# Optimization experiments

Hardware: AMD Instinct MI355X
Metric: run time of the kernel (lower is better)

## Reference

```python
import jax, jax.numpy as jnp
from jax import lax
import numpy as np

E = 16          # n_routed_experts
H = 2048        # hidden_size
I = 1408        # moe_intermediate_size
T = 2048        # tokens
K = 6           # top_k


def setup_inputs() -> dict:
    key = jax.random.key(0)
    k1, k2, k3, k4, k5 = jax.random.split(key, 5)
    hidden_states = jax.random.normal(k1, (T, H), dtype=jnp.float32)
    top_k_index = jax.random.randint(k2, (T, K), 0, E)
    top_k_weights = jax.random.uniform(k3, (T, K), dtype=jnp.float32)
    gate_up_proj = jax.random.normal(k4, (E, 2 * I, H), dtype=jnp.float32) * 0.02
    down_proj = jax.random.normal(k5, (E, H, I), dtype=jnp.float32) * 0.02
    return {
        "hidden_states": hidden_states,
        "top_k_index": top_k_index,
        "top_k_weights": top_k_weights,
        "gate_up_proj": gate_up_proj,
        "down_proj": down_proj,
    }


def reference(hidden_states, top_k_index, top_k_weights, gate_up_proj, down_proj):
    # combine[t, e] = sum over k-slots of top_k_weights[t, k] where top_k_index[t, k] == e
    # (scatter-add handles duplicate expert picks identically to index_add_).
    n_tok = hidden_states.shape[0]
    n_exp = gate_up_proj.shape[0]
    combine = jnp.zeros((n_tok, n_exp), hidden_states.dtype)
    combine = combine.at[jnp.arange(n_tok)[:, None], top_k_index].add(top_k_weights)

    def expert_step(acc, params):
        gu, dn, c_e = params  # gu: [2I, H], dn: [H, I], c_e: [n_tok]
        gate, up = jnp.split(hidden_states @ gu.T, 2, axis=-1)  # each [n_tok, I]
        y = (jax.nn.silu(gate) * up) @ dn.T                     # [n_tok, H]
        return acc + y * c_e[:, None], None

    out, _ = lax.scan(
        expert_step,
        jnp.zeros_like(hidden_states),
        (gate_up_proj, down_proj, combine.T),
    )
    return out
```

## Files before the change

kernel.cpp:

```cpp
#include <hip/hip_runtime.h>
#include <hip/hip_bf16.h>
#include <cstdint>

#define T_TOK 2048
#define HD 2048
#define ID 1408
#define NE 16
#define TOPK 6

#define BM 256
#define BK 64
#define BN 32
#define NT1 44
#define NT2 64
#define GMAX 64

typedef __bf16 bf16x8 __attribute__((ext_vector_type(8)));
typedef float f32x4 __attribute__((ext_vector_type(4)));

typedef const __attribute__((address_space(1))) void* gas1_t;
typedef __attribute__((address_space(3))) void* las3_t;
#define GLDS16(g, l) __builtin_amdgcn_global_load_lds((gas1_t)(g), (las3_t)(l), 16, 0, 0)


__global__ void k_combine(const int* __restrict__ idx, const float* __restrict__ w,
                          float* __restrict__ combine) {
    int t = blockIdx.x * blockDim.x + threadIdx.x;
    if (t >= T_TOK) return;
    int ie[TOPK];
    float fw[TOPK];
#pragma unroll
    for (int k = 0; k < TOPK; k++) { ie[k] = idx[t * TOPK + k]; fw[k] = w[t * TOPK + k]; }
#pragma unroll
    for (int e = 0; e < NE; e++) {
        float s = 0.f;
#pragma unroll
        for (int k = 0; k < TOPK; k++) if (ie[k] == e) s += fw[k];
        combine[t * NE + e] = s;
    }
}

__global__ void k_lists(const float* __restrict__ combine, int* __restrict__ counts,
                        int* __restrict__ tok, float* __restrict__ wts) {
    int t = blockIdx.x * blockDim.x + threadIdx.x;
    if (t >= T_TOK) return;
    for (int e = 0; e < NE; e++) {
        float c = combine[t * NE + e];
        if (c != 0.0f) {
            int p = atomicAdd(&counts[e], 1);
            tok[e * T_TOK + p] = t;
            wts[e * T_TOK + p] = c;
        }
    }
}

__global__ void k_cvt(const float* __restrict__ x, __bf16* __restrict__ xb) {
    int i = (blockIdx.x * 256 + threadIdx.x) * 8;
    float4 a = *(const float4*)(x + i);
    float4 b = *(const float4*)(x + i + 4);
    bf16x8 o;
    o[0] = (__bf16)a.x; o[1] = (__bf16)a.y; o[2] = (__bf16)a.z; o[3] = (__bf16)a.w;
    o[4] = (__bf16)b.x; o[5] = (__bf16)b.y; o[6] = (__bf16)b.z; o[7] = (__bf16)b.w;
    *(bf16x8*)(xb + i) = o;
}


__device__ __forceinline__ int swz(int row, int cb) {
    return row * 128 + (cb ^ ((row & 7) << 4));
}

__device__ __forceinline__ bf16x8 ldfrag(const __bf16* base, int row, int cb) {
    return *(const bf16x8*)((const char*)base + swz(row, cb));
}

__device__ __forceinline__ void stage8(const float* __restrict__ src, char* lds,
                                       int row, int cb) {
    float4 f0 = ((const float4*)src)[0];
    float4 f1 = ((const float4*)src)[1];
    bf16x8 o;
    o[0] = (__bf16)f0.x; o[1] = (__bf16)f0.y; o[2] = (__bf16)f0.z; o[3] = (__bf16)f0.w;
    o[4] = (__bf16)f1.x; o[5] = (__bf16)f1.y; o[6] = (__bf16)f1.z; o[7] = (__bf16)f1.w;
    *(bf16x8*)(lds + swz(row, cb)) = o;
}

__device__ __forceinline__ bool decode_item(const int* __restrict__ counts, int it,
                                            int ntn, int& e, int& m, int& n, int& cnt) {
    int r = it;
    for (int ee = 0; ee < NE; ee++) {
        int c = counts[ee];
        int nm = (c + BM - 1) >> 8;
        int tot = nm * ntn;
        if (r < tot) { e = ee; m = r % nm; n = r / nm; cnt = c; return true; }
        r -= tot;
    }
    return false;
}


__global__ __launch_bounds__(256, 4) void k_gemm1(
    const __bf16* __restrict__ Xb, const float* __restrict__ gup,
    const int* __restrict__ counts, const int* __restrict__ tok,
    __bf16* __restrict__ act) {
    __shared__ __align__(16) __bf16 sA[BM * BK];
    __shared__ __align__(16) __bf16 sBg[BN * BK];
    __shared__ __align__(16) __bf16 sBu[BN * BK];

    int e, m, n, cnt;
    if (!decode_item(counts, blockIdx.x, NT1, e, m, n, cnt)) return;
    int m0 = m * BM;
    int n0 = n * BN;

    int tid = threadIdx.x;
    int lane = tid & 63;
    int wid = tid >> 6;
    int l15 = lane & 15, lh = lane >> 4;
    int csw = ((lane & 7) ^ ((lane >> 3) & 7)) * 8;

    const __bf16* pA[8];
#pragma unroll
    for (int j = 0; j < 8; j++) {
        int r = 64 * wid + 8 * j + (lane >> 3);
        int g = m0 + r;
        if (g >= cnt) g = cnt - 1;
        pA[j] = Xb + (size_t)tok[e * T_TOK + g] * HD + csw;
    }

    int br = tid >> 3, bc = tid & 7;
    const float* gbase = gup + (size_t)e * (2 * ID) * HD;
    const float* bgSrc = gbase + (size_t)(n0 + br) * HD + bc * 8;
    const float* buSrc = gbase + (size_t)(ID + n0 + br) * HD + bc * 8;

    f32x4 accg[4][2] = {};
    f32x4 accu[4][2] = {};

    for (int k0 = 0; k0 < HD; k0 += BK) {
        __syncthreads();
#pragma unroll
        for (int j = 0; j < 8; j++)
            GLDS16(pA[j] + k0, &sA[(64 * wid + 8 * j) * BK]);
        stage8(bgSrc + k0, (char*)sBg, br, bc * 16);
        stage8(buSrc + k0, (char*)sBu, br, bc * 16);
        __syncthreads();
#pragma unroll
        for (int kk = 0; kk < 2; kk++) {
            int cb = kk * 64 + lh * 16;
            bf16x8 a[4];
#pragma unroll
            for (int fm = 0; fm < 4; fm++)
                a[fm] = ldfrag(sA, wid * 64 + fm * 16 + l15, cb);
#pragma unroll
            for (int fn = 0; fn < 2; fn++) {
                bf16x8 bg = ldfrag(sBg, fn * 16 + l15, cb);
                bf16x8 bu = ldfrag(sBu, fn * 16 + l15, cb);
#pragma unroll
                for (int fm = 0; fm < 4; fm++) {
                    accg[fm][fn] = __builtin_amdgcn_mfma_f32_16x16x32_bf16(a[fm], bg, accg[fm][fn], 0, 0, 0);
                    accu[fm][fn] = __builtin_amdgcn_mfma_f32_16x16x32_bf16(a[fm], bu, accu[fm][fn], 0, 0, 0);
                }
            }
        }
    }

#pragma unroll
    for (int fm = 0; fm < 4; fm++) {
#pragma unroll
        for (int fn = 0; fn < 2; fn++) {
#pragma unroll
            for (int j = 0; j < 4; j++) {
                int mloc = wid * 64 + fm * 16 + lh * 4 + j;
                int g = m0 + mloc;
                if (g < cnt) {
                    float gv = accg[fm][fn][j];
                    float uv = accu[fm][fn][j];
                    float sv = gv * (1.0f / (1.0f + __expf(-gv)));
                    int nn = n0 + fn * 16 + l15;
                    act[((size_t)e * T_TOK + g) * ID + nn] = (__bf16)(sv * uv);
                }
            }
        }
    }
}


__global__ __launch_bounds__(256, 4) void k_gemm2(
    const __bf16* __restrict__ act, const float* __restrict__ dn,
    const int* __restrict__ counts, const int* __restrict__ tok,
    const float* __restrict__ wts, float* __restrict__ out) {
    __shared__ __align__(16) __bf16 sA[BM * BK];
    __shared__ __align__(16) __bf16 sB[BN * BK];
    __shared__ int tokLds[BM];
    __shared__ float wtLds[BM];

    int e, m, n, cnt;
    if (!decode_item(counts, blockIdx.x, NT2, e, m, n, cnt)) return;
    int m0 = m * BM;
    int n0 = n * BN;

    int tid = threadIdx.x;
    int lane = tid & 63;
    int wid = tid >> 6;
    int l15 = lane & 15, lh = lane >> 4;
    int csw = ((lane & 7) ^ ((lane >> 3) & 7)) * 8;

    if (tid < BM) {
        int g = m0 + tid;
        bool v = g < cnt;
        tokLds[tid] = v ? tok[e * T_TOK + g] : 0;
        wtLds[tid] = v ? wts[e * T_TOK + g] : 0.f;
    }

    const __bf16* pA[8];
#pragma unroll
    for (int j = 0; j < 8; j++) {
        int r = 64 * wid + 8 * j + (lane >> 3);
        int g = m0 + r;
        if (g >= cnt) g = cnt - 1;
        pA[j] = act + ((size_t)e * T_TOK + g) * ID + csw;
    }

    int br = tid >> 3, bc = tid & 7;
    const float* bSrc = dn + (size_t)e * HD * ID + (size_t)(n0 + br) * ID + bc * 8;

    f32x4 acc[4][2] = {};

    for (int k0 = 0; k0 < ID; k0 += BK) {
        __syncthreads();
#pragma unroll
        for (int j = 0; j < 8; j++)
            GLDS16(pA[j] + k0, &sA[(64 * wid + 8 * j) * BK]);
        stage8(bSrc + k0, (char*)sB, br, bc * 16);
        __syncthreads();
#pragma unroll
        for (int kk = 0; kk < 2; kk++) {
            int cb = kk * 64 + lh * 16;
            bf16x8 a[4];
#pragma unroll
            for (int fm = 0; fm < 4; fm++)
                a[fm] = ldfrag(sA, wid * 64 + fm * 16 + l15, cb);
#pragma unroll
            for (int fn = 0; fn < 2; fn++) {
                bf16x8 b = ldfrag(sB, fn * 16 + l15, cb);
#pragma unroll
                for (int fm = 0; fm < 4; fm++)
                    acc[fm][fn] = __builtin_amdgcn_mfma_f32_16x16x32_bf16(a[fm], b, acc[fm][fn], 0, 0, 0);
            }
        }
    }

    __syncthreads();
#pragma unroll
    for (int fm = 0; fm < 4; fm++) {
#pragma unroll
        for (int fn = 0; fn < 2; fn++) {
#pragma unroll
            for (int j = 0; j < 4; j++) {
                int mloc = wid * 64 + fm * 16 + lh * 4 + j;
                int g = m0 + mloc;
                if (g < cnt) {
                    float v = acc[fm][fn][j] * wtLds[mloc];
                    int nn = n0 + fn * 16 + l15;
                    atomicAdd(&out[(size_t)tokLds[mloc] * HD + nn], v);
                }
            }
        }
    }
}


extern "C" void kernel_launch(void* const* d_in, const int* in_sizes, int n_in,
                              void* d_out, int out_size, void* d_ws, size_t ws_size,
                              hipStream_t stream) {
    const float* hs = (const float*)d_in[0];
    const int* tki = (const int*)d_in[1];
    const float* tkw = (const float*)d_in[2];
    const float* gup = (const float*)d_in[3];
    const float* dnp = (const float*)d_in[4];
    float* out = (float*)d_out;

    char* p = (char*)d_ws;
    int* counts = (int*)p;      p += 256;
    float* combine = (float*)p; p += (size_t)T_TOK * NE * 4;
    int* tok = (int*)p;         p += (size_t)NE * T_TOK * 4;
    float* wts = (float*)p;     p += (size_t)NE * T_TOK * 4;
    __bf16* Xb = (__bf16*)p;    p += (size_t)T_TOK * HD * 2;
    __bf16* act = (__bf16*)p;

    hipMemsetAsync(counts, 0, 256, stream);
    hipMemsetAsync(d_out, 0, (size_t)T_TOK * HD * 4, stream);
    k_combine<<<T_TOK / 256, 256, 0, stream>>>(tki, tkw, combine);
    k_lists<<<T_TOK / 256, 256, 0, stream>>>(combine, counts, tok, wts);
    k_cvt<<<(T_TOK * HD / 8) / 256, 256, 0, stream>>>(hs, Xb);
    k_gemm1<<<dim3(GMAX * NT1), 256, 0, stream>>>(Xb, gup, counts, tok, act);
    k_gemm2<<<dim3(GMAX * NT2), 256, 0, stream>>>(act, dnp, counts, tok, wts, out);
}
```

Baseline: 463.8 us.

## Pre-convert expert weights to bf16 and stream them via direct LDS loads

Adds a pass that converts the fp32 gate_up and down weights to bf16 in workspace before each GEMM, when the workspace is large enough. The GEMMs can then load weights with global_load_lds instead of per-thread fp32 loads followed by conversion and LDS stores. The trade-off is an extra full read of fp32 weights plus a bf16 write (about 277 MB fp32 total), and the GEMM tiles re-read the bf16 copy once per 256-token tile. The old fp32 GEMM paths are kept as a fallback when the workspace is too small.

```diff
diff --git a/kernel.cpp b/kernel.cpp
--- a/kernel.cpp
+++ b/kernel.cpp
@@ -64,6 +64,19 @@
     *(bf16x8*)(xb + i) = o;
 }
 
+__global__ void k_cvtw(const float* __restrict__ src, __bf16* __restrict__ dst, int n8) {
+    int stride = gridDim.x * blockDim.x;
+    for (int i = blockIdx.x * blockDim.x + threadIdx.x; i < n8; i += stride) {
+        size_t o = (size_t)i * 8;
+        float4 a = *(const float4*)(src + o);
+        float4 b = *(const float4*)(src + o + 4);
+        bf16x8 v;
+        v[0] = (__bf16)a.x; v[1] = (__bf16)a.y; v[2] = (__bf16)a.z; v[3] = (__bf16)a.w;
+        v[4] = (__bf16)b.x; v[5] = (__bf16)b.y; v[6] = (__bf16)b.z; v[7] = (__bf16)b.w;
+        *(bf16x8*)(dst + o) = v;
+    }
+}
+
 
 __device__ __forceinline__ int swz(int row, int cb) {
     return row * 128 + (cb ^ ((row & 7) << 4));
@@ -97,8 +110,8 @@
 }
 
 
-__global__ __launch_bounds__(256, 4) void k_gemm1(
-    const __bf16* __restrict__ Xb, const float* __restrict__ gup,
+__global__ __launch_bounds__(256, 4) void k_gemm1_bf16(
+    const __bf16* __restrict__ Xb, const __bf16* __restrict__ wgu,
     const int* __restrict__ counts, const int* __restrict__ tok,
     __bf16* __restrict__ act) {
     __shared__ __align__(16) __bf16 sA[BM * BK];
@@ -125,10 +138,11 @@
         pA[j] = Xb + (size_t)tok[e * T_TOK + g] * HD + csw;
     }
 
-    int br = tid >> 3, bc = tid & 7;
-    const float* gbase = gup + (size_t)e * (2 * ID) * HD;
-    const float* bgSrc = gbase + (size_t)(n0 + br) * HD + bc * 8;
-    const float* buSrc = gbase + (size_t)(ID + n0 + br) * HD + bc * 8;
+    int brow = 8 * wid + (lane >> 3);
+    int bsw = ((lane & 7) ^ (lane >> 3)) * 8;
+    const __bf16* wbase = wgu + (size_t)e * (2 * ID) * HD;
+    const __bf16* pBg = wbase + (size_t)(n0 + brow) * HD + bsw;
+    const __bf16* pBu = wbase + (size_t)(ID + n0 + brow) * HD + bsw;
 
     f32x4 accg[4][2] = {};
     f32x4 accu[4][2] = {};
@@ -138,8 +152,8 @@
 #pragma unroll
         for (int j = 0; j < 8; j++)
             GLDS16(pA[j] + k0, &sA[(64 * wid + 8 * j) * BK]);
-        stage8(bgSrc + k0, (char*)sBg, br, bc * 16);
-        stage8(buSrc + k0, (char*)sBu, br, bc * 16);
+        GLDS16(pBg + k0, &sBg[wid * 512]);
+        GLDS16(pBu + k0, &sBu[wid * 512]);
         __syncthreads();
 #pragma unroll
         for (int kk = 0; kk < 2; kk++) {
@@ -182,7 +196,178 @@
 }
 
 
-__global__ __launch_bounds__(256, 4) void k_gemm2(
+__global__ __launch_bounds__(256, 4) void k_gemm1_f32(
+    const __bf16* __restrict__ Xb, const float* __restrict__ gup,
+    const int* __restrict__ counts, const int* __restrict__ tok,
+    __bf16* __restrict__ act) {
+    __shared__ __align__(16) __bf16 sA[BM * BK];
+    __shared__ __align__(16) __bf16 sBg[BN * BK];
+    __shared__ __align__(16) __bf16 sBu[BN * BK];
+
+    int e, m, n, cnt;
+    if (!decode_item(counts, blockIdx.x, NT1, e, m, n, cnt)) return;
+    int m0 = m * BM;
+    int n0 = n * BN;
+
+    int tid = threadIdx.x;
+    int lane = tid & 63;
+    int wid = tid >> 6;
+    int l15 = lane & 15, lh = lane >> 4;
+    int csw = ((lane & 7) ^ ((lane >> 3) & 7)) * 8;
+
+    const __bf16* pA[8];
+#pragma unroll
+    for (int j = 0; j < 8; j++) {
+        int r = 64 * wid + 8 * j + (lane >> 3);
+        int g = m0 + r;
+        if (g >= cnt) g = cnt - 1;
+        pA[j] = Xb + (size_t)tok[e * T_TOK + g] * HD + csw;
+    }
+
+    int br = tid >> 3, bc = tid & 7;
+    const float* gbase = gup + (size_t)e * (2 * ID) * HD;
+    const float* bgSrc = gbase + (size_t)(n0 + br) * HD + bc * 8;
+    const float* buSrc = gbase + (size_t)(ID + n0 + br) * HD + bc * 8;
+
+    f32x4 accg[4][2] = {};
+    f32x4 accu[4][2] = {};
+
+    for (int k0 = 0; k0 < HD; k0 += BK) {
+        __syncthreads();
+#pragma unroll
+        for (int j = 0; j < 8; j++)
+            GLDS16(pA[j] + k0, &sA[(64 * wid + 8 * j) * BK]);
+        stage8(bgSrc + k0, (char*)sBg, br, bc * 16);
+        stage8(buSrc + k0, (char*)sBu, br, bc * 16);
+        __syncthreads();
+#pragma unroll
+        for (int kk = 0; kk < 2; kk++) {
+            int cb = kk * 64 + lh * 16;
+            bf16x8 a[4];
+#pragma unroll
+            for (int fm = 0; fm < 4; fm++)
+                a[fm] = ldfrag(sA, wid * 64 + fm * 16 + l15, cb);
+#pragma unroll
+            for (int fn = 0; fn < 2; fn++) {
+                bf16x8 bg = ldfrag(sBg, fn * 16 + l15, cb);
+                bf16x8 bu = ldfrag(sBu, fn * 16 + l15, cb);
+#pragma unroll
+                for (int fm = 0; fm < 4; fm++) {
+                    accg[fm][fn] = __builtin_amdgcn_mfma_f32_16x16x32_bf16(a[fm], bg, accg[fm][fn], 0, 0, 0);
+                    accu[fm][fn] = __builtin_amdgcn_mfma_f32_16x16x32_bf16(a[fm], bu, accu[fm][fn], 0, 0, 0);
+                }
+            }
+        }
+    }
+
+#pragma unroll
+    for (int fm = 0; fm < 4; fm++) {
+#pragma unroll
+        for (int fn = 0; fn < 2; fn++) {
+#pragma unroll
+            for (int j = 0; j < 4; j++) {
+                int mloc = wid * 64 + fm * 16 + lh * 4 + j;
+                int g = m0 + mloc;
+                if (g < cnt) {
+                    float gv = accg[fm][fn][j];
+                    float uv = accu[fm][fn][j];
+                    float sv = gv * (1.0f / (1.0f + __expf(-gv)));
+                    int nn = n0 + fn * 16 + l15;
+                    act[((size_t)e * T_TOK + g) * ID + nn] = (__bf16)(sv * uv);
+                }
+            }
+        }
+    }
+}
+
+
+__global__ __launch_bounds__(256, 4) void k_gemm2_bf16(
+    const __bf16* __restrict__ act, const __bf16* __restrict__ wdn,
+    const int* __restrict__ counts, const int* __restrict__ tok,
+    const float* __restrict__ wts, float* __restrict__ out) {
+    __shared__ __align__(16) __bf16 sA[BM * BK];
+    __shared__ __align__(16) __bf16 sB[BN * BK];
+    __shared__ int tokLds[BM];
+    __shared__ float wtLds[BM];
+
+    int e, m, n, cnt;
+    if (!decode_item(counts, blockIdx.x, NT2, e, m, n, cnt)) return;
+    int m0 = m * BM;
+    int n0 = n * BN;
+
+    int tid = threadIdx.x;
+    int lane = tid & 63;
+    int wid = tid >> 6;
+    int l15 = lane & 15, lh = lane >> 4;
+    int csw = ((lane & 7) ^ ((lane >> 3) & 7)) * 8;
+
+    if (tid < BM) {
+        int g = m0 + tid;
+        bool v = g < cnt;
+        tokLds[tid] = v ? tok[e * T_TOK + g] : 0;
+        wtLds[tid] = v ? wts[e * T_TOK + g] : 0.f;
+    }
+
+    const __bf16* pA[8];
+#pragma unroll
+    for (int j = 0; j < 8; j++) {
+        int r = 64 * wid + 8 * j + (lane >> 3);
+        int g = m0 + r;
+        if (g >= cnt) g = cnt - 1;
+        pA[j] = act + ((size_t)e * T_TOK + g) * ID + csw;
+    }
+
+    int brow = 8 * wid + (lane >> 3);
+    int bsw = ((lane & 7) ^ (lane >> 3)) * 8;
+    const __bf16* pB = wdn + ((size_t)e * HD + (n0 + brow)) * ID + bsw;
+
+    f32x4 acc[4][2] = {};
+
+    for (int k0 = 0; k0 < ID; k0 += BK) {
+        __syncthreads();
+#pragma unroll
+        for (int j = 0; j < 8; j++)
+            GLDS16(pA[j] + k0, &sA[(64 * wid + 8 * j) * BK]);
+        GLDS16(pB + k0, &sB[wid * 512]);
+        __syncthreads();
+#pragma unroll
+        for (int kk = 0; kk < 2; kk++) {
+            int cb = kk * 64 + lh * 16;
+            bf16x8 a[4];
+#pragma unroll
+            for (int fm = 0; fm < 4; fm++)
+                a[fm] = ldfrag(sA, wid * 64 + fm * 16 + l15, cb);
+#pragma unroll
+            for (int fn = 0; fn < 2; fn++) {
+                bf16x8 b = ldfrag(sB, fn * 16 + l15, cb);
+#pragma unroll
+                for (int fm = 0; fm < 4; fm++)
+                    acc[fm][fn] = __builtin_amdgcn_mfma_f32_16x16x32_bf16(a[fm], b, acc[fm][fn], 0, 0, 0);
+            }
+        }
+    }
+
+    __syncthreads();
+#pragma unroll
+    for (int fm = 0; fm < 4; fm++) {
+#pragma unroll
+        for (int fn = 0; fn < 2; fn++) {
+#pragma unroll
+            for (int j = 0; j < 4; j++) {
+                int mloc = wid * 64 + fm * 16 + lh * 4 + j;
+                int g = m0 + mloc;
+                if (g < cnt) {
+                    float v = acc[fm][fn][j] * wtLds[mloc];
+                    int nn = n0 + fn * 16 + l15;
+                    atomicAdd(&out[(size_t)tokLds[mloc] * HD + nn], v);
+                }
+            }
+        }
+    }
+}
+
+
+__global__ __launch_bounds__(256, 4) void k_gemm2_f32(
     const __bf16* __restrict__ act, const float* __restrict__ dn,
     const int* __restrict__ counts, const int* __restrict__ tok,
     const float* __restrict__ wts, float* __restrict__ out) {
@@ -277,19 +462,40 @@
     const float* dnp = (const float*)d_in[4];
     float* out = (float*)d_out;
 
+    const size_t nGU = (size_t)NE * (2 * ID) * HD;
+    const size_t nDN = (size_t)NE * HD * ID;
+
     char* p = (char*)d_ws;
     int* counts = (int*)p;      p += 256;
     float* combine = (float*)p; p += (size_t)T_TOK * NE * 4;
     int* tok = (int*)p;         p += (size_t)NE * T_TOK * 4;
     float* wts = (float*)p;     p += (size_t)NE * T_TOK * 4;
     __bf16* Xb = (__bf16*)p;    p += (size_t)T_TOK * HD * 2;
-    __bf16* act = (__bf16*)p;
+    __bf16* act = (__bf16*)p;   p += (size_t)NE * T_TOK * ID * 2;
+    size_t used_base = (size_t)(p - (char*)d_ws);
+    __bf16* wgu = (__bf16*)p;
+    __bf16* wdn = (__bf16*)(p + nGU * 2);
+
+    bool cvt_gu = ws_size >= used_base + nGU * 2;
+    bool cvt_dn = ws_size >= used_base + nGU * 2 + nDN * 2;
 
     hipMemsetAsync(counts, 0, 256, stream);
     hipMemsetAsync(d_out, 0, (size_t)T_TOK * HD * 4, stream);
     k_combine<<<T_TOK / 256, 256, 0, stream>>>(tki, tkw, combine);
     k_lists<<<T_TOK / 256, 256, 0, stream>>>(combine, counts, tok, wts);
     k_cvt<<<(T_TOK * HD / 8) / 256, 256, 0, stream>>>(hs, Xb);
-    k_gemm1<<<dim3(GMAX * NT1), 256, 0, stream>>>(Xb, gup, counts, tok, act);
-    k_gemm2<<<dim3(GMAX * NT2), 256, 0, stream>>>(act, dnp, counts, tok, wts, out);
-}
+
+    if (cvt_gu) {
+        k_cvtw<<<2048, 256, 0, stream>>>(gup, wgu, (int)(nGU / 8));
+        k_gemm1_bf16<<<dim3(GMAX * NT1), 256, 0, stream>>>(Xb, wgu, counts, tok, act);
+    } else {
+        k_gemm1_f32<<<dim3(GMAX * NT1), 256, 0, stream>>>(Xb, gup, counts, tok, act);
+    }
+
+    if (cvt_dn) {
+        k_cvtw<<<2048, 256, 0, stream>>>(dnp, wdn, (int)(nDN / 8));
+        k_gemm2_bf16<<<dim3(GMAX * NT2), 256, 0, stream>>>(act, wdn, counts, tok, wts, out);
+    } else {
+        k_gemm2_f32<<<dim3(GMAX * NT2), 256, 0, stream>>>(act, dnp, counts, tok, wts, out);
+    }
+}
```

New measurement: 507.8 us. 9.5% more time.

## Software-pipeline weight loads with double-buffered LDS in both expert GEMMs

Applied to the files above, without the earlier changes.

Both grouped GEMM kernels now prefetch the next K-tile of fp32 weights into registers while computing the current tile, and stage the B tiles into double-buffered LDS. Explicit waitcnt and raw barriers replace __syncthreads, so the A tile load is issued right after compute. gemm1 launch bounds drop to 3 waves per SIMD to allow more registers. gemm2 also drops the LDS token/weight table and reads tok and wts directly in the epilogue. The hand-written waitcnt counts are fragile, and the lower occupancy hint may reduce latency hiding.

```diff
diff --git a/kernel.cpp b/kernel.cpp
--- a/kernel.cpp
+++ b/kernel.cpp
@@ -21,6 +21,14 @@
 typedef const __attribute__((address_space(1))) void* gas1_t;
 typedef __attribute__((address_space(3))) void* las3_t;
 #define GLDS16(g, l) __builtin_amdgcn_global_load_lds((gas1_t)(g), (las3_t)(l), 16, 0, 0)
+
+__device__ __forceinline__ void bar() {
+    asm volatile("" ::: "memory");
+    __builtin_amdgcn_s_barrier();
+    asm volatile("" ::: "memory");
+}
+#define WAITV(N) asm volatile("s_waitcnt vmcnt(" #N ")" ::: "memory")
+#define WAITL0   asm volatile("s_waitcnt lgkmcnt(0)" ::: "memory")
 
 
 __global__ void k_combine(const int* __restrict__ idx, const float* __restrict__ w,
@@ -73,10 +81,7 @@
     return *(const bf16x8*)((const char*)base + swz(row, cb));
 }
 
-__device__ __forceinline__ void stage8(const float* __restrict__ src, char* lds,
-                                       int row, int cb) {
-    float4 f0 = ((const float4*)src)[0];
-    float4 f1 = ((const float4*)src)[1];
+__device__ __forceinline__ void stage8v(char* lds, int row, int cb, float4 f0, float4 f1) {
     bf16x8 o;
     o[0] = (__bf16)f0.x; o[1] = (__bf16)f0.y; o[2] = (__bf16)f0.z; o[3] = (__bf16)f0.w;
     o[4] = (__bf16)f1.x; o[5] = (__bf16)f1.y; o[6] = (__bf16)f1.z; o[7] = (__bf16)f1.w;
@@ -97,13 +102,13 @@
 }
 
 
-__global__ __launch_bounds__(256, 4) void k_gemm1(
+__global__ __launch_bounds__(256, 3) void k_gemm1(
     const __bf16* __restrict__ Xb, const float* __restrict__ gup,
     const int* __restrict__ counts, const int* __restrict__ tok,
     __bf16* __restrict__ act) {
     __shared__ __align__(16) __bf16 sA[BM * BK];
-    __shared__ __align__(16) __bf16 sBg[BN * BK];
-    __shared__ __align__(16) __bf16 sBu[BN * BK];
+    __shared__ __align__(16) __bf16 sBg[2][BN * BK];
+    __shared__ __align__(16) __bf16 sBu[2][BN * BK];
 
     int e, m, n, cnt;
     if (!decode_item(counts, blockIdx.x, NT1, e, m, n, cnt)) return;
@@ -133,14 +138,31 @@
     f32x4 accg[4][2] = {};
     f32x4 accu[4][2] = {};
 
-    for (int k0 = 0; k0 < HD; k0 += BK) {
-        __syncthreads();
-#pragma unroll
-        for (int j = 0; j < 8; j++)
-            GLDS16(pA[j] + k0, &sA[(64 * wid + 8 * j) * BK]);
-        stage8(bgSrc + k0, (char*)sBg, br, bc * 16);
-        stage8(buSrc + k0, (char*)sBu, br, bc * 16);
-        __syncthreads();
+    const int NT = HD / BK;
+
+    float4 g0 = ((const float4*)bgSrc)[0], g1 = ((const float4*)bgSrc)[1];
+    float4 u0 = ((const float4*)buSrc)[0], u1 = ((const float4*)buSrc)[1];
+#pragma unroll
+    for (int j = 0; j < 8; j++)
+        GLDS16(pA[j], &sA[(64 * wid + 8 * j) * BK]);
+    stage8v((char*)sBg[0], br, bc * 16, g0, g1);
+    stage8v((char*)sBu[0], br, bc * 16, u0, u1);
+    WAITL0;
+    bar();
+
+    for (int k = 0; k < NT; k++) {
+        int cur = k & 1, nxt = cur ^ 1;
+        int kn = (k + 1 < NT) ? (k + 1) : k;
+        {
+            const float* bg = bgSrc + kn * BK;
+            const float* bu = buSrc + kn * BK;
+            g0 = ((const float4*)bg)[0]; g1 = ((const float4*)bg)[1];
+            u0 = ((const float4*)bu)[0]; u1 = ((const float4*)bu)[1];
+        }
+        WAITV(4);
+        bar();
+        const __bf16* sBgc = sBg[cur];
+        const __bf16* sBuc = sBu[cur];
 #pragma unroll
         for (int kk = 0; kk < 2; kk++) {
             int cb = kk * 64 + lh * 16;
@@ -150,14 +172,23 @@
                 a[fm] = ldfrag(sA, wid * 64 + fm * 16 + l15, cb);
 #pragma unroll
             for (int fn = 0; fn < 2; fn++) {
-                bf16x8 bg = ldfrag(sBg, fn * 16 + l15, cb);
-                bf16x8 bu = ldfrag(sBu, fn * 16 + l15, cb);
+                bf16x8 bg = ldfrag(sBgc, fn * 16 + l15, cb);
+                bf16x8 bu = ldfrag(sBuc, fn * 16 + l15, cb);
 #pragma unroll
                 for (int fm = 0; fm < 4; fm++) {
                     accg[fm][fn] = __builtin_amdgcn_mfma_f32_16x16x32_bf16(a[fm], bg, accg[fm][fn], 0, 0, 0);
                     accu[fm][fn] = __builtin_amdgcn_mfma_f32_16x16x32_bf16(a[fm], bu, accu[fm][fn], 0, 0, 0);
                 }
             }
+        }
+        stage8v((char*)sBg[nxt], br, bc * 16, g0, g1);
+        stage8v((char*)sBu[nxt], br, bc * 16, u0, u1);
+        WAITL0;
+        bar();
+        if (k + 1 < NT) {
+#pragma unroll
+            for (int j = 0; j < 8; j++)
+                GLDS16(pA[j] + (k + 1) * BK, &sA[(64 * wid + 8 * j) * BK]);
         }
     }
 
@@ -187,9 +218,7 @@
     const int* __restrict__ counts, const int* __restrict__ tok,
     const float* __restrict__ wts, float* __restrict__ out) {
     __shared__ __align__(16) __bf16 sA[BM * BK];
-    __shared__ __align__(16) __bf16 sB[BN * BK];
-    __shared__ int tokLds[BM];
-    __shared__ float wtLds[BM];
+    __shared__ __align__(16) __bf16 sB[2][BN * BK];
 
     int e, m, n, cnt;
     if (!decode_item(counts, blockIdx.x, NT2, e, m, n, cnt)) return;
@@ -202,13 +231,6 @@
     int l15 = lane & 15, lh = lane >> 4;
     int csw = ((lane & 7) ^ ((lane >> 3) & 7)) * 8;
 
-    if (tid < BM) {
-        int g = m0 + tid;
-        bool v = g < cnt;
-        tokLds[tid] = v ? tok[e * T_TOK + g] : 0;
-        wtLds[tid] = v ? wts[e * T_TOK + g] : 0.f;
-    }
-
     const __bf16* pA[8];
 #pragma unroll
     for (int j = 0; j < 8; j++) {
@@ -223,13 +245,26 @@
 
     f32x4 acc[4][2] = {};
 
-    for (int k0 = 0; k0 < ID; k0 += BK) {
-        __syncthreads();
-#pragma unroll
-        for (int j = 0; j < 8; j++)
-            GLDS16(pA[j] + k0, &sA[(64 * wid + 8 * j) * BK]);
-        stage8(bSrc + k0, (char*)sB, br, bc * 16);
-        __syncthreads();
+    const int NT = ID / BK;
+
+    float4 b0 = ((const float4*)bSrc)[0], b1 = ((const float4*)bSrc)[1];
+#pragma unroll
+    for (int j = 0; j < 8; j++)
+        GLDS16(pA[j], &sA[(64 * wid + 8 * j) * BK]);
+    stage8v((char*)sB[0], br, bc * 16, b0, b1);
+    WAITL0;
+    bar();
+
+    for (int k = 0; k < NT; k++) {
+        int cur = k & 1, nxt = cur ^ 1;
+        int kn = (k + 1 < NT) ? (k + 1) : k;
+        {
+            const float* bs = bSrc + kn * BK;
+            b0 = ((const float4*)bs)[0]; b1 = ((const float4*)bs)[1];
+        }
+        WAITV(2);
+        bar();
+        const __bf16* sBc = sB[cur];
 #pragma unroll
         for (int kk = 0; kk < 2; kk++) {
             int cb = kk * 64 + lh * 16;
@@ -239,27 +274,35 @@
                 a[fm] = ldfrag(sA, wid * 64 + fm * 16 + l15, cb);
 #pragma unroll
             for (int fn = 0; fn < 2; fn++) {
-                bf16x8 b = ldfrag(sB, fn * 16 + l15, cb);
+                bf16x8 b = ldfrag(sBc, fn * 16 + l15, cb);
 #pragma unroll
                 for (int fm = 0; fm < 4; fm++)
                     acc[fm][fn] = __builtin_amdgcn_mfma_f32_16x16x32_bf16(a[fm], b, acc[fm][fn], 0, 0, 0);
             }
         }
-    }
-
-    __syncthreads();
+        stage8v((char*)sB[nxt], br, bc * 16, b0, b1);
+        WAITL0;
+        bar();
+        if (k + 1 < NT) {
+#pragma unroll
+            for (int j = 0; j < 8; j++)
+                GLDS16(pA[j] + (k + 1) * BK, &sA[(64 * wid + 8 * j) * BK]);
+        }
+    }
+
 #pragma unroll
     for (int fm = 0; fm < 4; fm++) {
 #pragma unroll
-        for (int fn = 0; fn < 2; fn++) {
-#pragma unroll
-            for (int j = 0; j < 4; j++) {
-                int mloc = wid * 64 + fm * 16 + lh * 4 + j;
-                int g = m0 + mloc;
-                if (g < cnt) {
-                    float v = acc[fm][fn][j] * wtLds[mloc];
+        for (int j = 0; j < 4; j++) {
+            int mloc = wid * 64 + fm * 16 + lh * 4 + j;
+            int g = m0 + mloc;
+            if (g < cnt) {
+                int t = tok[e * T_TOK + g];
+                float w = wts[e * T_TOK + g];
+#pragma unroll
+                for (int fn = 0; fn < 2; fn++) {
                     int nn = n0 + fn * 16 + l15;
-                    atomicAdd(&out[(size_t)tokLds[mloc] * HD + nn], v);
+                    atomicAdd(&out[(size_t)t * HD + nn], acc[fm][fn][j] * w);
                 }
             }
         }
```

Result: slower. 552.6 us (+19.2%).

## Double-buffer LDS tiles with BK=32 and prefetch next tile in both GEMMs

Applied to the files above, without the earlier changes.

Both expert GEMM kernels now use two LDS buffers with a K-tile of 32. The next tile's activation rows are issued via global_load_lds and the weight floats are loaded into registers before the current tile's MFMAs, then converted and stored after them, leaving one barrier per iteration. This is meant to hide global load latency behind matrix math. The swizzle is adapted to the 64-byte rows, and the down-projection epilogue reads token and weight indices straight from global memory instead of staging them in LDS. The cost is twice as many loop iterations with half the math per barrier, plus extra registers for the prefetched values.

```diff
diff --git a/kernel.cpp b/kernel.cpp
--- a/kernel.cpp
+++ b/kernel.cpp
@@ -9,7 +9,7 @@
 #define TOPK 6
 
 #define BM 256
-#define BK 64
+#define BK 32
 #define BN 32
 #define NT1 44
 #define NT2 64
@@ -65,22 +65,19 @@
 }
 
 
-__device__ __forceinline__ int swz(int row, int cb) {
-    return row * 128 + (cb ^ ((row & 7) << 4));
-}
-
-__device__ __forceinline__ bf16x8 ldfrag(const __bf16* base, int row, int cb) {
-    return *(const bf16x8*)((const char*)base + swz(row, cb));
-}
-
-__device__ __forceinline__ void stage8(const float* __restrict__ src, char* lds,
-                                       int row, int cb) {
-    float4 f0 = ((const float4*)src)[0];
-    float4 f1 = ((const float4*)src)[1];
+__device__ __forceinline__ int swz32(int row, int cb) {
+    return row * 64 + (cb ^ (((row >> 1) & 3) << 4));
+}
+
+__device__ __forceinline__ bf16x8 ldfrag32(const __bf16* base, int row, int cb) {
+    return *(const bf16x8*)((const char*)base + swz32(row, cb));
+}
+
+__device__ __forceinline__ void stage8v32(char* lds, int row, int q, float4 f0, float4 f1) {
     bf16x8 o;
     o[0] = (__bf16)f0.x; o[1] = (__bf16)f0.y; o[2] = (__bf16)f0.z; o[3] = (__bf16)f0.w;
     o[4] = (__bf16)f1.x; o[5] = (__bf16)f1.y; o[6] = (__bf16)f1.z; o[7] = (__bf16)f1.w;
-    *(bf16x8*)(lds + swz(row, cb)) = o;
+    *(bf16x8*)(lds + swz32(row, q << 4)) = o;
 }
 
 __device__ __forceinline__ bool decode_item(const int* __restrict__ counts, int it,
@@ -101,9 +98,9 @@
     const __bf16* __restrict__ Xb, const float* __restrict__ gup,
     const int* __restrict__ counts, const int* __restrict__ tok,
     __bf16* __restrict__ act) {
-    __shared__ __align__(16) __bf16 sA[BM * BK];
-    __shared__ __align__(16) __bf16 sBg[BN * BK];
-    __shared__ __align__(16) __bf16 sBu[BN * BK];
+    __shared__ __align__(16) __bf16 sA[2][BM * BK];
+    __shared__ __align__(16) __bf16 sBg[2][BN * BK];
+    __shared__ __align__(16) __bf16 sBu[2][BN * BK];
 
     int e, m, n, cnt;
     if (!decode_item(counts, blockIdx.x, NT1, e, m, n, cnt)) return;
@@ -114,51 +111,76 @@
     int lane = tid & 63;
     int wid = tid >> 6;
     int l15 = lane & 15, lh = lane >> 4;
-    int csw = ((lane & 7) ^ ((lane >> 3) & 7)) * 8;
-
-    const __bf16* pA[8];
-#pragma unroll
-    for (int j = 0; j < 8; j++) {
-        int r = 64 * wid + 8 * j + (lane >> 3);
+
+    const __bf16* pA[4];
+    int csw = ((lane & 3) ^ ((lane >> 3) & 3)) * 8;
+#pragma unroll
+    for (int j = 0; j < 4; j++) {
+        int r = 64 * wid + 16 * j + (lane >> 2);
         int g = m0 + r;
         if (g >= cnt) g = cnt - 1;
         pA[j] = Xb + (size_t)tok[e * T_TOK + g] * HD + csw;
     }
 
-    int br = tid >> 3, bc = tid & 7;
+    int t4 = tid & 127;
+    int brow = t4 >> 2, bq = t4 & 3;
     const float* gbase = gup + (size_t)e * (2 * ID) * HD;
-    const float* bgSrc = gbase + (size_t)(n0 + br) * HD + bc * 8;
-    const float* buSrc = gbase + (size_t)(ID + n0 + br) * HD + bc * 8;
+    const float* bSrc = (tid < 128)
+        ? gbase + (size_t)(n0 + brow) * HD + bq * 8
+        : gbase + (size_t)(ID + n0 + brow) * HD + bq * 8;
 
     f32x4 accg[4][2] = {};
     f32x4 accu[4][2] = {};
 
-    for (int k0 = 0; k0 < HD; k0 += BK) {
+    const int NT = HD / BK;
+
+    {
+        float4 b0 = ((const float4*)bSrc)[0], b1 = ((const float4*)bSrc)[1];
+#pragma unroll
+        for (int j = 0; j < 4; j++)
+            GLDS16(pA[j], &sA[0][(64 * wid + 16 * j) * BK]);
+        char* dst = (tid < 128) ? (char*)sBg[0] : (char*)sBu[0];
+        stage8v32(dst, brow, bq, b0, b1);
+    }
+    __syncthreads();
+
+    for (int k = 0; k < NT; k++) {
+        int cur = k & 1, nxt = cur ^ 1;
+        bool pf = (k + 1 < NT);
+        float4 b0, b1;
+        if (pf) {
+            int k0 = (k + 1) * BK;
+#pragma unroll
+            for (int j = 0; j < 4; j++)
+                GLDS16(pA[j] + k0, &sA[nxt][(64 * wid + 16 * j) * BK]);
+            const float* bs = bSrc + k0;
+            b0 = ((const float4*)bs)[0]; b1 = ((const float4*)bs)[1];
+        }
+
+        const __bf16* sAc = sA[cur];
+        const __bf16* sBgc = sBg[cur];
+        const __bf16* sBuc = sBu[cur];
+        int cb = lh * 16;
+        bf16x8 a[4];
+#pragma unroll
+        for (int fm = 0; fm < 4; fm++)
+            a[fm] = ldfrag32(sAc, wid * 64 + fm * 16 + l15, cb);
+#pragma unroll
+        for (int fn = 0; fn < 2; fn++) {
+            bf16x8 bg = ldfrag32(sBgc, fn * 16 + l15, cb);
+            bf16x8 bu = ldfrag32(sBuc, fn * 16 + l15, cb);
+#pragma unroll
+            for (int fm = 0; fm < 4; fm++) {
+                accg[fm][fn] = __builtin_amdgcn_mfma_f32_16x16x32_bf16(a[fm], bg, accg[fm][fn], 0, 0, 0);
+                accu[fm][fn] = __builtin_amdgcn_mfma_f32_16x16x32_bf16(a[fm], bu, accu[fm][fn], 0, 0, 0);
+            }
+        }
+
+        if (pf) {
+            char* dst = (tid < 128) ? (char*)sBg[nxt] : (char*)sBu[nxt];
+            stage8v32(dst, brow, bq, b0, b1);
+        }
         __syncthreads();
-#pragma unroll
-        for (int j = 0; j < 8; j++)
-            GLDS16(pA[j] + k0, &sA[(64 * wid + 8 * j) * BK]);
-        stage8(bgSrc + k0, (char*)sBg, br, bc * 16);
-        stage8(buSrc + k0, (char*)sBu, br, bc * 16);
-        __syncthreads();
-#pragma unroll
-        for (int kk = 0; kk < 2; kk++) {
-            int cb = kk * 64 + lh * 16;
-            bf16x8 a[4];
-#pragma unroll
-            for (int fm = 0; fm < 4; fm++)
-                a[fm] = ldfrag(sA, wid * 64 + fm * 16 + l15, cb);
-#pragma unroll
-            for (int fn = 0; fn < 2; fn++) {
-                bf16x8 bg = ldfrag(sBg, fn * 16 + l15, cb);
-                bf16x8 bu = ldfrag(sBu, fn * 16 + l15, cb);
-#pragma unroll
-                for (int fm = 0; fm < 4; fm++) {
-                    accg[fm][fn] = __builtin_amdgcn_mfma_f32_16x16x32_bf16(a[fm], bg, accg[fm][fn], 0, 0, 0);
-                    accu[fm][fn] = __builtin_amdgcn_mfma_f32_16x16x32_bf16(a[fm], bu, accu[fm][fn], 0, 0, 0);
-                }
-            }
-        }
     }
 
 #pragma unroll
@@ -186,10 +208,8 @@
     const __bf16* __restrict__ act, const float* __restrict__ dn,
     const int* __restrict__ counts, const int* __restrict__ tok,
     const float* __restrict__ wts, float* __restrict__ out) {
-    __shared__ __align__(16) __bf16 sA[BM * BK];
-    __shared__ __align__(16) __bf16 sB[BN * BK];
-    __shared__ int tokLds[BM];
-    __shared__ float wtLds[BM];
+    __shared__ __align__(16) __bf16 sA[2][BM * BK];
+    __shared__ __align__(16) __bf16 sB[2][BN * BK];
 
     int e, m, n, cnt;
     if (!decode_item(counts, blockIdx.x, NT2, e, m, n, cnt)) return;
@@ -200,66 +220,82 @@
     int lane = tid & 63;
     int wid = tid >> 6;
     int l15 = lane & 15, lh = lane >> 4;
-    int csw = ((lane & 7) ^ ((lane >> 3) & 7)) * 8;
-
-    if (tid < BM) {
-        int g = m0 + tid;
-        bool v = g < cnt;
-        tokLds[tid] = v ? tok[e * T_TOK + g] : 0;
-        wtLds[tid] = v ? wts[e * T_TOK + g] : 0.f;
-    }
-
-    const __bf16* pA[8];
-#pragma unroll
-    for (int j = 0; j < 8; j++) {
-        int r = 64 * wid + 8 * j + (lane >> 3);
+
+    const __bf16* pA[4];
+    int csw = ((lane & 3) ^ ((lane >> 3) & 3)) * 8;
+#pragma unroll
+    for (int j = 0; j < 4; j++) {
+        int r = 64 * wid + 16 * j + (lane >> 2);
         int g = m0 + r;
         if (g >= cnt) g = cnt - 1;
         pA[j] = act + ((size_t)e * T_TOK + g) * ID + csw;
     }
 
-    int br = tid >> 3, bc = tid & 7;
-    const float* bSrc = dn + (size_t)e * HD * ID + (size_t)(n0 + br) * ID + bc * 8;
+    int t4 = tid & 127;
+    int brow = t4 >> 2, bq = t4 & 3;
+    const float* bSrc = dn + (size_t)e * HD * ID + (size_t)(n0 + brow) * ID + bq * 8;
 
     f32x4 acc[4][2] = {};
 
-    for (int k0 = 0; k0 < ID; k0 += BK) {
+    const int NT = ID / BK;
+
+    {
+        float4 b0, b1;
+        if (tid < 128) { b0 = ((const float4*)bSrc)[0]; b1 = ((const float4*)bSrc)[1]; }
+#pragma unroll
+        for (int j = 0; j < 4; j++)
+            GLDS16(pA[j], &sA[0][(64 * wid + 16 * j) * BK]);
+        if (tid < 128) stage8v32((char*)sB[0], brow, bq, b0, b1);
+    }
+    __syncthreads();
+
+    for (int k = 0; k < NT; k++) {
+        int cur = k & 1, nxt = cur ^ 1;
+        bool pf = (k + 1 < NT);
+        float4 b0, b1;
+        if (pf) {
+            int k0 = (k + 1) * BK;
+#pragma unroll
+            for (int j = 0; j < 4; j++)
+                GLDS16(pA[j] + k0, &sA[nxt][(64 * wid + 16 * j) * BK]);
+            if (tid < 128) {
+                const float* bs = bSrc + k0;
+                b0 = ((const float4*)bs)[0]; b1 = ((const float4*)bs)[1];
+            }
+        }
+
+        const __bf16* sAc = sA[cur];
+        const __bf16* sBc = sB[cur];
+        int cb = lh * 16;
+        bf16x8 a[4];
+#pragma unroll
+        for (int fm = 0; fm < 4; fm++)
+            a[fm] = ldfrag32(sAc, wid * 64 + fm * 16 + l15, cb);
+#pragma unroll
+        for (int fn = 0; fn < 2; fn++) {
+            bf16x8 b = ldfrag32(sBc, fn * 16 + l15, cb);
+#pragma unroll
+            for (int fm = 0; fm < 4; fm++)
+                acc[fm][fn] = __builtin_amdgcn_mfma_f32_16x16x32_bf16(a[fm], b, acc[fm][fn], 0, 0, 0);
+        }
+
+        if (pf && tid < 128) stage8v32((char*)sB[nxt], brow, bq, b0, b1);
         __syncthreads();
-#pragma unroll
-        for (int j = 0; j < 8; j++)
-            GLDS16(pA[j] + k0, &sA[(64 * wid + 8 * j) * BK]);
-        stage8(bSrc + k0, (char*)sB, br, bc * 16);
-        __syncthreads();
-#pragma unroll
-        for (int kk = 0; kk < 2; kk++) {
-            int cb = kk * 64 + lh * 16;
-            bf16x8 a[4];
-#pragma unroll
-            for (int fm = 0; fm < 4; fm++)
-                a[fm] = ldfrag(sA, wid * 64 + fm * 16 + l15, cb);
-#pragma unroll
-            for (int fn = 0; fn < 2; fn++) {
-                bf16x8 b = ldfrag(sB, fn * 16 + l15, cb);
-#pragma unroll
-                for (int fm = 0; fm < 4; fm++)
-                    acc[fm][fn] = __builtin_amdgcn_mfma_f32_16x16x32_bf16(a[fm], b, acc[fm][fn], 0, 0, 0);
-            }
-        }
-    }
-
-    __syncthreads();
+    }
+
 #pragma unroll
     for (int fm = 0; fm < 4; fm++) {
 #pragma unroll
-        for (int fn = 0; fn < 2; fn++) {
-#pragma unroll
-            for (int j = 0; j < 4; j++) {
-                int mloc = wid * 64 + fm * 16 + lh * 4 + j;
-                int g = m0 + mloc;
-                if (g < cnt) {
-                    float v = acc[fm][fn][j] * wtLds[mloc];
+        for (int j = 0; j < 4; j++) {
+            int mloc = wid * 64 + fm * 16 + lh * 4 + j;
+            int g = m0 + mloc;
+            if (g < cnt) {
+                int t = tok[e * T_TOK + g];
+                float w = wts[e * T_TOK + g];
+#pragma unroll
+                for (int fn = 0; fn < 2; fn++) {
                     int nn = n0 + fn * 16 + l15;
-                    atomicAdd(&out[(size_t)tokLds[mloc] * HD + nn], v);
+                    atomicAdd(&out[(size_t)t * HD + nn], acc[fm][fn][j] * w);
                 }
             }
         }
```

Result: slower. 583.8 us (+25.9%).
